# Kernel optimization log

Hardware: AMD Instinct MI355X
Metric: run time of the kernel (lower is better)

## Reference

```python
import jax, jax.numpy as jnp
import numpy as np

B, S, H, NH = 2, 2048, 1024, 16
HD = H // NH  # head dim = 64


def setup_inputs() -> dict:
    key = jax.random.key(0)
    k_in, k_q, k_kv, k_o = jax.random.split(key, 4)
    scale = 0.02
    return {
        "inputs": jax.random.normal(k_in, (B, S, H), dtype=jnp.float32),
        "Wq": jax.random.normal(k_q, (H, H), dtype=jnp.float32) * scale,
        "bq": jnp.zeros((H,), dtype=jnp.float32),
        "Wkv": jax.random.normal(k_kv, (H, 2 * H), dtype=jnp.float32) * scale,
        "bkv": jnp.zeros((2 * H,), dtype=jnp.float32),
        "Wo": jax.random.normal(k_o, (H, H), dtype=jnp.float32) * scale,
        "bo": jnp.zeros((H,), dtype=jnp.float32),
    }


def reference(inputs, Wq, bq, Wkv, bkv, Wo, bo):
    b, s, h = inputs.shape
    q = inputs @ Wq + bq                      # [B,S,H]
    kv = inputs @ Wkv + bkv                   # [B,S,2H]
    k, v = kv[..., :h], kv[..., h:]           # each [B,S,H]
    q = q.reshape(b, s, NH, HD)
    k = k.reshape(b, s, NH, HD)
    v = v.reshape(b, s, NH, HD)
    inv_sqrt_d = jnp.asarray(1.0 / np.sqrt(HD), dtype=inputs.dtype)
    scores = jnp.einsum("bqhd,bkhd->bhqk", q, k) * inv_sqrt_d  # [B,NH,S,S]
    probs = jax.nn.softmax(scores, axis=-1)
    attended = jnp.einsum("bhqk,bkhd->bqhd", probs, v)         # [B,S,NH,HD]
    attended = attended.reshape(b, s, h)
    return attended @ Wo + bo
```

## Files before the change

kernel.cpp:

```cpp
#include <hip/hip_runtime.h>
#include <cstdint>

typedef __bf16 bf16;
typedef __attribute__((ext_vector_type(8))) __bf16 bf16x8;
typedef __attribute__((ext_vector_type(4))) __bf16 bf16v4;
typedef __attribute__((ext_vector_type(4))) float f32x4;
typedef __attribute__((ext_vector_type(16))) float f32x16;

#define MFMA16(a, b, c) __builtin_amdgcn_mfma_f32_16x16x32_bf16((a), (b), (c), 0, 0, 0)
#define MFMA32(a, b, c) __builtin_amdgcn_mfma_f32_32x32x16_bf16((a), (b), (c), 0, 0, 0)

#define BATCH 2
#define SLEN 2048
#define HDIM 1024
#define NHEAD 16
#define HEADD 64
#define MROWS (BATCH * SLEN)

#define CEXP 0.1803368801f

typedef __attribute__((address_space(3))) void lds_void;
typedef const __attribute__((address_space(1))) void glb_void;
__device__ __forceinline__ void load_lds16(const bf16* g, bf16* l) {
    __builtin_amdgcn_global_load_lds((glb_void*)g, (lds_void*)l, 16, 0, 0);
}

__global__ __launch_bounds__(256) void prep_kernel(const float* __restrict__ X,
                                                   const float* __restrict__ Wq,
                                                   const float* __restrict__ Wkv,
                                                   const float* __restrict__ Wo,
                                                   const float* __restrict__ bq,
                                                   const float* __restrict__ bkv,
                                                   bf16* __restrict__ Xbf,
                                                   bf16* __restrict__ WqkvT,
                                                   bf16* __restrict__ WoT,
                                                   float* __restrict__ bqkv) {
    const int blk = blockIdx.x;
    const int tid = threadIdx.x;
    if (blk < 4096) {
        int i = (blk * 256 + tid) * 4;
        float4 v = *(const float4*)&X[i];
        bf16v4 o;
        o[0] = (bf16)v.x; o[1] = (bf16)v.y; o[2] = (bf16)v.z; o[3] = (bf16)v.w;
        *(bf16v4*)&Xbf[i] = o;
        return;
    }
    if (blk < 8192) {
        const float* in; bf16* out; int C, id;
        if (blk < 5120)      { in = Wq;  out = WqkvT;                C = 1024; id = blk - 4096; }
        else if (blk < 7168) { in = Wkv; out = WqkvT + 1024 * 1024;  C = 2048; id = blk - 5120; }
        else                 { in = Wo;  out = WoT;                  C = 1024; id = blk - 7168; }
        const int R = 1024;
        const int nbx = C / 32;
        const int j0 = (id % nbx) * 32, i0 = (id / nbx) * 32;
        const int tx = tid & 31, ty = tid >> 5;
        __shared__ float t[32][33];
        for (int r = ty; r < 32; r += 8)
            t[r][tx] = in[(size_t)(i0 + r) * C + j0 + tx];
        __syncthreads();
        for (int r = ty; r < 32; r += 8)
            out[(size_t)(j0 + r) * R + i0 + tx] = (bf16)t[tx][r];
        return;
    }
    int i = (blk - 8192) * 256 + tid;
    if (i < 3072) bqkv[i] = (i < 1024) ? bq[i] : bkv[i - 1024];
}

template <int BM, int BN, int EPI>
__global__ __launch_bounds__(256) void gemm2_kernel(const bf16* __restrict__ A,
                                                    const bf16* __restrict__ BT,
                                                    const float* __restrict__ bias,
                                                    bf16* __restrict__ oQ,
                                                    bf16* __restrict__ oK,
                                                    bf16* __restrict__ oVT,
                                                    float* __restrict__ oF, int K) {
    constexpr int WM = BM / 2, WN = BN / 2;
    constexpr int MT = WM / 16, NT = WN / 16;

    const int tid = threadIdx.x;
    const int lane = tid & 63, wid = tid >> 6;
    const int l15 = lane & 15, quad = lane >> 4;
    const int wm = (wid >> 1) * WM, wn = (wid & 1) * WN;
    const int m0 = blockIdx.y * BM, n0 = blockIdx.x * BN;

    __shared__ bf16 As[BM * 32];
    __shared__ bf16 Bs[BN * 32];

    f32x4 acc[MT][NT] = {};

    const bf16* Ag = A + (size_t)m0 * K;
    const bf16* Bg = BT + (size_t)n0 * K;
    const int arow = lane >> 2, acol = (lane & 3) * 8;

    for (int k0 = 0; k0 < K; k0 += 32) {
#pragma unroll
        for (int t = 0; t < BM / 64; ++t) {
            int tt = t * 4 + wid;
            load_lds16(Ag + (size_t)(tt * 16 + arow) * K + k0 + acol, &As[tt * 512]);
        }
#pragma unroll
        for (int t = 0; t < BN / 64; ++t) {
            int tt = t * 4 + wid;
            load_lds16(Bg + (size_t)(tt * 16 + arow) * K + k0 + acol, &Bs[tt * 512]);
        }
        __syncthreads();

        bf16x8 af[MT], bfr[NT];
#pragma unroll
        for (int i = 0; i < MT; ++i)
            af[i] = *(const bf16x8*)&As[(wm + i * 16 + l15) * 32 + quad * 8];
#pragma unroll
        for (int j = 0; j < NT; ++j)
            bfr[j] = *(const bf16x8*)&Bs[(wn + j * 16 + l15) * 32 + quad * 8];
#pragma unroll
        for (int i = 0; i < MT; ++i)
#pragma unroll
            for (int j = 0; j < NT; ++j)
                acc[i][j] = MFMA16(af[i], bfr[j], acc[i][j]);
        __syncthreads();
    }

#pragma unroll
    for (int i = 0; i < MT; ++i) {
#pragma unroll
        for (int j = 0; j < NT; ++j) {
            const int mb = m0 + wm + i * 16 + quad * 4;
            const int n = n0 + wn + j * 16 + l15;
            const float bv = bias[n];
            if (EPI == 2) {
                float* o = oF + (size_t)mb * 1024 + n;
#pragma unroll
                for (int r = 0; r < 4; ++r) o[(size_t)r * 1024] = acc[i][j][r] + bv;
            } else if (n0 < 1024) {
#pragma unroll
                for (int r = 0; r < 4; ++r)
                    oQ[(size_t)(mb + r) * 1024 + n] = (bf16)((acc[i][j][r] + bv) * CEXP);
            } else if (n0 < 2048) {
#pragma unroll
                for (int r = 0; r < 4; ++r)
                    oK[(size_t)(mb + r) * 1024 + (n - 1024)] = (bf16)(acc[i][j][r] + bv);
            } else {
                const int hd = n - 2048;
                const int bb = mb >> 11, ss = mb & 2047;
                bf16v4 pk;
#pragma unroll
                for (int r = 0; r < 4; ++r) pk[r] = (bf16)(acc[i][j][r] + bv);
                *(bf16v4*)&oVT[((size_t)(bb << 10) + hd) * 2048 + ss] = pk;
            }
        }
    }
}

__global__ __launch_bounds__(256, 4) void attn7_kernel(const bf16* __restrict__ Q,
                                                       const bf16* __restrict__ K,
                                                       const bf16* __restrict__ VT,
                                                       bf16* __restrict__ O) {
    const int bid = blockIdx.x;
    const int xcd = bid & 7, j = bid >> 3;
    const int bh = xcd * 4 + (j >> 5);
    const int q0 = (j & 31) * 64;
    const int b = bh >> 4, head = bh & 15;
    const int tid = threadIdx.x;
    const int lane = tid & 63, wid = tid >> 6;
    const int l31 = lane & 31, hh = lane >> 5;
    const int qgroup = wid & 1, khalf = wid >> 1;

    __shared__ union SMem {
        struct { bf16 Ks[128 * 64]; bf16 VTs[64 * 128]; } t;
        float Xs[8192];
    } sm;
    bf16* Ks = sm.t.Ks;
    bf16* VTs = sm.t.VTs;

    const int qw = q0 + qgroup * 32;
    bf16x8 qf[4];
#pragma unroll
    for (int kd = 0; kd < 4; ++kd)
        qf[kd] = *(const bf16x8*)&Q[(size_t)(b * SLEN + qw + l31) * HDIM +
                                    head * 64 + kd * 16 + hh * 8];

    f32x16 o_acc[2] = {};
    float lp0 = 0.f, lp1 = 0.f, lp2 = 0.f, lp3 = 0.f;

    const bf16* Kg = K + (size_t)b * SLEN * HDIM + head * 64;
    const bf16* Vg = VT + (size_t)bh * 64 * SLEN;

    const int r8 = lane >> 3, p8 = lane & 7;
    const int r16 = lane >> 4, p16 = lane & 15;
    const int kb = khalf * 64;
    const int sw7 = l31 & 7, sw15 = l31 & 15;

    for (int kt = 0; kt < 16; ++kt) {
        const int k0 = kt * 128;
#pragma unroll
        for (int pass = 0; pass < 4; ++pass) {
            const int rbk = pass * 32 + wid * 8;
            load_lds16(Kg + (size_t)(k0 + rbk + r8) * HDIM + ((p8 ^ ((rbk + r8) & 7)) * 8),
                       &Ks[rbk * 64]);
            const int rbv = pass * 16 + wid * 4;
            load_lds16(Vg + (size_t)(rbv + r16) * SLEN + k0 + ((p16 ^ ((rbv + r16) & 15)) * 8),
                       &VTs[rbv * 128]);
        }
        __syncthreads();

        f32x16 sacc[2] = {};
#pragma unroll
        for (int kd = 0; kd < 4; ++kd)
#pragma unroll
            for (int m = 0; m < 2; ++m) {
                const int key = kb + m * 32 + l31;
                const int c = (kd * 2 + hh) ^ sw7;
                bf16x8 kf = *(const bf16x8*)&Ks[key * 64 + c * 8];
                sacc[m] = MFMA32(kf, qf[kd], sacc[m]);
            }

#pragma unroll
        for (int m = 0; m < 2; ++m)
#pragma unroll
            for (int g = 0; g < 4; ++g) {
                float p0 = __builtin_amdgcn_exp2f(sacc[m][g * 4 + 0]);
                float p1 = __builtin_amdgcn_exp2f(sacc[m][g * 4 + 1]);
                float p2 = __builtin_amdgcn_exp2f(sacc[m][g * 4 + 2]);
                float p3 = __builtin_amdgcn_exp2f(sacc[m][g * 4 + 3]);
                lp0 += p0; lp1 += p1; lp2 += p2; lp3 += p3;
                sacc[m][g * 4 + 0] = p0; sacc[m][g * 4 + 1] = p1;
                sacc[m][g * 4 + 2] = p2; sacc[m][g * 4 + 3] = p3;
            }

#pragma unroll
        for (int s = 0; s < 4; ++s) {
            const int m = s >> 1, base = 8 * (s & 1);
            bf16v4 lo4, hi4;
#pragma unroll
            for (int r = 0; r < 4; ++r) {
                lo4[r] = (bf16)sacc[m][base + r];
                hi4[r] = (bf16)sacc[m][base + 4 + r];
            }
            uint2 lo = __builtin_bit_cast(uint2, lo4);
            uint2 hi = __builtin_bit_cast(uint2, hi4);
            unsigned s0 = hh ? lo.x : hi.x;
            unsigned s1 = hh ? lo.y : hi.y;
            unsigned r0 = __shfl_xor(s0, 32, 64);
            unsigned r1 = __shfl_xor(s1, 32, 64);
            uint4 f;
            f.x = hh ? r0 : lo.x;
            f.y = hh ? r1 : lo.y;
            f.z = hh ? hi.x : r0;
            f.w = hh ? hi.y : r1;
            bf16x8 pf = __builtin_bit_cast(bf16x8, f);
#pragma unroll
            for (int dt = 0; dt < 2; ++dt) {
                const int d = dt * 32 + l31;
                const int cc = (khalf * 8 + s * 2 + hh) ^ sw15;
                bf16x8 vf = *(const bf16x8*)&VTs[d * 128 + cc * 8];
                o_acc[dt] = MFMA32(vf, pf, o_acc[dt]);
            }
        }
        __syncthreads();
    }

    float l_lane = (lp0 + lp1) + (lp2 + lp3);
    l_lane += __shfl_xor(l_lane, 32, 64);

    float* Xs = sm.Xs;
    if (khalf == 1) {
        float* w = Xs + qgroup * 2304 + lane * 36;
#pragma unroll
        for (int mt = 0; mt < 2; ++mt)
#pragma unroll
            for (int g = 0; g < 4; ++g) {
                f32x4 v = {o_acc[mt][g * 4 + 0], o_acc[mt][g * 4 + 1],
                           o_acc[mt][g * 4 + 2], o_acc[mt][g * 4 + 3]};
                *(f32x4*)&w[mt * 16 + g * 4] = v;
            }
        if (hh == 0) Xs[4608 + qgroup * 32 + l31] = l_lane;
    }
    __syncthreads();
    if (khalf == 0) {
        const float* w = Xs + qgroup * 2304 + lane * 36;
        const float l_full = l_lane + Xs[4608 + qgroup * 32 + l31];
        const float inv = 1.f / l_full;
        bf16* orow = O + (size_t)(b * SLEN + qw + l31) * HDIM + head * 64;
#pragma unroll
        for (int mt = 0; mt < 2; ++mt)
#pragma unroll
            for (int g = 0; g < 4; ++g) {
                f32x4 v = *(const f32x4*)&w[mt * 16 + g * 4];
                bf16v4 pk;
#pragma unroll
                for (int r = 0; r < 4; ++r)
                    pk[r] = (bf16)((o_acc[mt][g * 4 + r] + v[r]) * inv);
                *(bf16v4*)&orow[mt * 32 + g * 8 + 4 * hh] = pk;
            }
    }
}

extern "C" void kernel_launch(void* const* d_in, const int* in_sizes, int n_in,
                              void* d_out, int out_size, void* d_ws, size_t ws_size,
                              hipStream_t stream) {
    const float* X   = (const float*)d_in[0];
    const float* Wq  = (const float*)d_in[1];
    const float* bq  = (const float*)d_in[2];
    const float* Wkv = (const float*)d_in[3];
    const float* bkv = (const float*)d_in[4];
    const float* Wo  = (const float*)d_in[5];
    const float* bo  = (const float*)d_in[6];
    float* out = (float*)d_out;

    char* ws = (char*)d_ws;
    bf16* Xbf   = (bf16*)(ws);
    bf16* WqkvT = (bf16*)(ws + (8ull << 20));
    bf16* WoT   = (bf16*)(ws + (14ull << 20));
    float* bqkv = (float*)(ws + (16ull << 20));
    bf16* Qbf   = (bf16*)(ws + (17ull << 20));
    bf16* Kbf   = (bf16*)(ws + (25ull << 20));
    bf16* VTbf  = (bf16*)(ws + (33ull << 20));
    bf16* Abf   = (bf16*)(ws + (41ull << 20));

    prep_kernel<<<8204, 256, 0, stream>>>(X, Wq, Wkv, Wo, bq, bkv, Xbf, WqkvT, WoT, bqkv);

    gemm2_kernel<128, 128, 1><<<dim3(3072 / 128, MROWS / 128), 256, 0, stream>>>(
        Xbf, WqkvT, bqkv, Qbf, Kbf, VTbf, nullptr, 1024);

    attn7_kernel<<<1024, 256, 0, stream>>>(Qbf, Kbf, VTbf, Abf);

    gemm2_kernel<128, 64, 2><<<dim3(1024 / 64, MROWS / 128), 256, 0, stream>>>(
        Abf, WoT, bo, nullptr, nullptr, nullptr, out, 1024);
}
```

Measured before the change: 205.1 us.

## Load K/V fragments directly from global into registers, dropping LDS staging

The attention kernel no longer stages K and V^T tiles through shared memory with barriers. Each wave now owns 32 query rows and walks all keys itself, loading K and V fragments straight from global memory into registers with software double-buffering across 64-key halves. This removes the cross-wave split-K reduction through LDS and halves the grid to 512 blocks of 128 queries. In exchange, each wave issues its own global loads with no sharing between waves in a block, which increases L2/global traffic and register pressure, and the launch bound no longer requests 4 blocks per CU.

Measured after the change: 267.0 us. 1.3x slower.

```diff
diff --git a/kernel.cpp b/kernel.cpp
--- a/kernel.cpp
+++ b/kernel.cpp
@@ -151,28 +151,20 @@
     }
 }
 
-__global__ __launch_bounds__(256, 4) void attn7_kernel(const bf16* __restrict__ Q,
-                                                       const bf16* __restrict__ K,
-                                                       const bf16* __restrict__ VT,
-                                                       bf16* __restrict__ O) {
+__global__ __launch_bounds__(256) void attn8_kernel(const bf16* __restrict__ Q,
+                                                    const bf16* __restrict__ K,
+                                                    const bf16* __restrict__ VT,
+                                                    bf16* __restrict__ O) {
     const int bid = blockIdx.x;
     const int xcd = bid & 7, j = bid >> 3;
-    const int bh = xcd * 4 + (j >> 5);
-    const int q0 = (j & 31) * 64;
+    const int bh = xcd * 4 + (j >> 4);
+    const int q0 = (j & 15) * 128;
     const int b = bh >> 4, head = bh & 15;
     const int tid = threadIdx.x;
     const int lane = tid & 63, wid = tid >> 6;
     const int l31 = lane & 31, hh = lane >> 5;
-    const int qgroup = wid & 1, khalf = wid >> 1;
-
-    __shared__ union SMem {
-        struct { bf16 Ks[128 * 64]; bf16 VTs[64 * 128]; } t;
-        float Xs[8192];
-    } sm;
-    bf16* Ks = sm.t.Ks;
-    bf16* VTs = sm.t.VTs;
-
-    const int qw = q0 + qgroup * 32;
+
+    const int qw = q0 + wid * 32;
     bf16x8 qf[4];
 #pragma unroll
     for (int kd = 0; kd < 4; ++kd)
@@ -182,37 +174,34 @@
     f32x16 o_acc[2] = {};
     float lp0 = 0.f, lp1 = 0.f, lp2 = 0.f, lp3 = 0.f;
 
-    const bf16* Kg = K + (size_t)b * SLEN * HDIM + head * 64;
-    const bf16* Vg = VT + (size_t)bh * 64 * SLEN;
-
-    const int r8 = lane >> 3, p8 = lane & 7;
-    const int r16 = lane >> 4, p16 = lane & 15;
-    const int kb = khalf * 64;
-    const int sw7 = l31 & 7, sw15 = l31 & 15;
-
-    for (int kt = 0; kt < 16; ++kt) {
-        const int k0 = kt * 128;
-#pragma unroll
-        for (int pass = 0; pass < 4; ++pass) {
-            const int rbk = pass * 32 + wid * 8;
-            load_lds16(Kg + (size_t)(k0 + rbk + r8) * HDIM + ((p8 ^ ((rbk + r8) & 7)) * 8),
-                       &Ks[rbk * 64]);
-            const int rbv = pass * 16 + wid * 4;
-            load_lds16(Vg + (size_t)(rbv + r16) * SLEN + k0 + ((p16 ^ ((rbv + r16) & 15)) * 8),
-                       &VTs[rbv * 128]);
-        }
-        __syncthreads();
-
+    const bf16* kbase = K + (size_t)b * SLEN * HDIM + head * 64 +
+                        (size_t)l31 * HDIM + hh * 8;
+    const bf16* vbase = VT + (size_t)bh * 64 * SLEN + (size_t)l31 * SLEN + hh * 8;
+
+    bf16x8 kfA[8], kfB[8], vf[8];
+
+    auto loadK = [&](bf16x8* kf, int k0) {
+#pragma unroll
+        for (int kd = 0; kd < 4; ++kd)
+#pragma unroll
+            for (int m = 0; m < 2; ++m)
+                kf[kd * 2 + m] = *(const bf16x8*)&kbase[(size_t)(k0 + m * 32) * HDIM + kd * 16];
+    };
+    auto loadV = [&](int k0) {
+#pragma unroll
+        for (int s = 0; s < 4; ++s)
+#pragma unroll
+            for (int dt = 0; dt < 2; ++dt)
+                vf[s * 2 + dt] = *(const bf16x8*)&vbase[(size_t)dt * 32 * SLEN + k0 + s * 16];
+    };
+
+    auto half = [&](const bf16x8* kf) {
         f32x16 sacc[2] = {};
 #pragma unroll
         for (int kd = 0; kd < 4; ++kd)
 #pragma unroll
-            for (int m = 0; m < 2; ++m) {
-                const int key = kb + m * 32 + l31;
-                const int c = (kd * 2 + hh) ^ sw7;
-                bf16x8 kf = *(const bf16x8*)&Ks[key * 64 + c * 8];
-                sacc[m] = MFMA32(kf, qf[kd], sacc[m]);
-            }
+            for (int m = 0; m < 2; ++m)
+                sacc[m] = MFMA32(kf[kd * 2 + m], qf[kd], sacc[m]);
 
 #pragma unroll
         for (int m = 0; m < 2; ++m)
@@ -249,50 +238,36 @@
             f.w = hh ? hi.y : r1;
             bf16x8 pf = __builtin_bit_cast(bf16x8, f);
 #pragma unroll
-            for (int dt = 0; dt < 2; ++dt) {
-                const int d = dt * 32 + l31;
-                const int cc = (khalf * 8 + s * 2 + hh) ^ sw15;
-                bf16x8 vf = *(const bf16x8*)&VTs[d * 128 + cc * 8];
-                o_acc[dt] = MFMA32(vf, pf, o_acc[dt]);
-            }
-        }
-        __syncthreads();
+            for (int dt = 0; dt < 2; ++dt)
+                o_acc[dt] = MFMA32(vf[s * 2 + dt], pf, o_acc[dt]);
+        }
+    };
+
+    loadK(kfA, 0);
+#pragma unroll 1
+    for (int kt2 = 0; kt2 < 16; ++kt2) {
+        const int k0 = kt2 * 128;
+        loadV(k0);
+        loadK(kfB, k0 + 64);
+        half(kfA);
+        loadV(k0 + 64);
+        if (kt2 < 15) loadK(kfA, k0 + 128);
+        half(kfB);
     }
 
     float l_lane = (lp0 + lp1) + (lp2 + lp3);
-    l_lane += __shfl_xor(l_lane, 32, 64);
-
-    float* Xs = sm.Xs;
-    if (khalf == 1) {
-        float* w = Xs + qgroup * 2304 + lane * 36;
-#pragma unroll
-        for (int mt = 0; mt < 2; ++mt)
-#pragma unroll
-            for (int g = 0; g < 4; ++g) {
-                f32x4 v = {o_acc[mt][g * 4 + 0], o_acc[mt][g * 4 + 1],
-                           o_acc[mt][g * 4 + 2], o_acc[mt][g * 4 + 3]};
-                *(f32x4*)&w[mt * 16 + g * 4] = v;
-            }
-        if (hh == 0) Xs[4608 + qgroup * 32 + l31] = l_lane;
-    }
-    __syncthreads();
-    if (khalf == 0) {
-        const float* w = Xs + qgroup * 2304 + lane * 36;
-        const float l_full = l_lane + Xs[4608 + qgroup * 32 + l31];
-        const float inv = 1.f / l_full;
-        bf16* orow = O + (size_t)(b * SLEN + qw + l31) * HDIM + head * 64;
-#pragma unroll
-        for (int mt = 0; mt < 2; ++mt)
-#pragma unroll
-            for (int g = 0; g < 4; ++g) {
-                f32x4 v = *(const f32x4*)&w[mt * 16 + g * 4];
-                bf16v4 pk;
-#pragma unroll
-                for (int r = 0; r < 4; ++r)
-                    pk[r] = (bf16)((o_acc[mt][g * 4 + r] + v[r]) * inv);
-                *(bf16v4*)&orow[mt * 32 + g * 8 + 4 * hh] = pk;
-            }
-    }
+    const float l_full = l_lane + __shfl_xor(l_lane, 32, 64);
+    const float inv = 1.f / l_full;
+    bf16* orow = O + (size_t)(b * SLEN + qw + l31) * HDIM + head * 64;
+#pragma unroll
+    for (int dt = 0; dt < 2; ++dt)
+#pragma unroll
+        for (int g = 0; g < 4; ++g) {
+            bf16v4 pk;
+#pragma unroll
+            for (int r = 0; r < 4; ++r) pk[r] = (bf16)(o_acc[dt][g * 4 + r] * inv);
+            *(bf16v4*)&orow[dt * 32 + g * 8 + 4 * hh] = pk;
+        }
 }
 
 extern "C" void kernel_launch(void* const* d_in, const int* in_sizes, int n_in,
@@ -322,7 +297,7 @@
     gemm2_kernel<128, 128, 1><<<dim3(3072 / 128, MROWS / 128), 256, 0, stream>>>(
         Xbf, WqkvT, bqkv, Qbf, Kbf, VTbf, nullptr, 1024);
 
-    attn7_kernel<<<1024, 256, 0, stream>>>(Qbf, Kbf, VTbf, Abf);
+    attn8_kernel<<<512, 256, 0, stream>>>(Qbf, Kbf, VTbf, Abf);
 
     gemm2_kernel<128, 64, 2><<<dim3(1024 / 64, MROWS / 128), 256, 0, stream>>>(
         Abf, WoT, bo, nullptr, nullptr, nullptr, out, 1024);
```
